# Optimization experiments

Hardware: AMD Instinct MI355X
Metric: run time of the kernel (lower is better)

Reference implementation:

```python
import jax, jax.numpy as jnp
import numpy as np

B, S, D_IN, D_OUT = 4, 4096, 768, 768

def setup_inputs() -> dict:
    key = jax.random.key(0)
    k1, k2, k3, k4 = jax.random.split(key, 4)
    x = jax.random.normal(k1, (B, S, D_IN), dtype=jnp.float32)
    # Stored as [d_in, d_out]; torch Linear computes x @ W.T with W [d_out, d_in],
    # which is equivalent to x @ W_here for a fresh random init.
    Wq = jax.random.normal(k2, (D_IN, D_OUT), dtype=jnp.float32) * (1.0 / np.sqrt(D_IN))
    Wk = jax.random.normal(k3, (D_IN, D_OUT), dtype=jnp.float32) * (1.0 / np.sqrt(D_IN))
    Wv = jax.random.normal(k4, (D_IN, D_OUT), dtype=jnp.float32) * (1.0 / np.sqrt(D_IN))
    return {"x": x, "Wq": Wq, "Wk": Wk, "Wv": Wv}

def reference(x, Wq, Wk, Wv):
    # x: [B, S, d_in]
    q = jnp.einsum('bsi,io->bso', x, Wq)  # [B, S, d_out]
    k = jnp.einsum('bsi,io->bso', x, Wk)
    v = jnp.einsum('bsi,io->bso', x, Wv)
    scale = 1.0 / jnp.sqrt(jnp.asarray(q.shape[-1], dtype=q.dtype))
    scores = jnp.einsum('bqd,bkd->bqk', q, k)  # [B, S, S]
    S_len = scores.shape[-1]
    causal = jnp.tril(jnp.ones((S_len, S_len), dtype=bool))  # True = keep
    scores = jnp.where(causal[None, :, :], scores, -jnp.inf)
    weights = jax.nn.softmax(scores * scale, axis=-1)
    # dropout p=0.0 -> identity
    return jnp.einsum('bqk,bkd->bqd', weights, v)
```

## Files before the change

### kernel.cpp

```cpp
#include <hip/hip_runtime.h>

typedef __attribute__((ext_vector_type(8))) short short8;
typedef __attribute__((ext_vector_type(4))) float f32x4;
typedef unsigned short u16;

#define MFMA_BF16 __builtin_amdgcn_mfma_f32_16x16x32_bf16
#define S_BARRIER()  asm volatile("s_barrier" ::: "memory")
#define WAIT_LGKM0() asm volatile("s_waitcnt lgkmcnt(0)" ::: "memory")
#define WAIT_VM(n)   asm volatile("s_waitcnt vmcnt(" #n ")" ::: "memory")

__device__ __forceinline__ u16 f2bf(float f) {
    unsigned int u = __builtin_bit_cast(unsigned int, f);
    u = (u + 0x7FFFu + ((u >> 16) & 1u)) >> 16;
    return (u16)u;
}

__device__ __forceinline__ void gl_lds16(const void* g, void* l) {
    __builtin_amdgcn_global_load_lds(
        (const __attribute__((address_space(1))) unsigned int*)g,
        (__attribute__((address_space(3))) unsigned int*)l, 16, 0, 0);
}

constexpr int D = 768;
constexpr int S = 4096;
constexpr float SCALE = 0.03608439182435161f;

__device__ __forceinline__ void tri_decode(int t, int& i, int& j) {
    i = (int)((sqrtf(8.0f * t + 1.0f) - 1.0f) * 0.5f);
    while ((i + 1) * (i + 2) / 2 <= t) ++i;
    while (i * (i + 1) / 2 > t) --i;
    j = t - i * (i + 1) / 2;
}

template<int NCH>
__device__ __forceinline__ void stage64(const u16* __restrict__ g, u16* lds, int kcol, int tid) {
    #pragma unroll
    for (int i = 0; i < NCH; ++i) {
        const int ch = i * 512 + tid;
        const int row = ch >> 3, c = ch & 7;
        const int cs = c ^ (row & 7);
        gl_lds16(g + (size_t)row * 768 + kcol + cs * 8, lds + ch * 8);
    }
}
__device__ __forceinline__ short8 ldsfrag(const u16* p, int row, int ks, int lane) {
    const int cs = (ks * 4 + (lane >> 4)) ^ (row & 7);
    return *reinterpret_cast<const short8*>(p + row * 64 + cs * 8);
}

__global__ __launch_bounds__(256)
void conv_x(const float* __restrict__ x, u16* __restrict__ xb) {
    const size_t i = ((size_t)blockIdx.x * 256 + threadIdx.x) * 4;
    const float4 v = *reinterpret_cast<const float4*>(x + i);
    ushort4 o;
    o.x = f2bf(v.x); o.y = f2bf(v.y); o.z = f2bf(v.z); o.w = f2bf(v.w);
    *reinterpret_cast<ushort4*>(xb + i) = o;
}

__global__ __launch_bounds__(256)
void conv_wt(const float* __restrict__ Wq, const float* __restrict__ Wk,
             const float* __restrict__ Wv, u16* __restrict__ WT) {
    __shared__ float t[64][65];
    const int tid = threadIdx.x;
    const int k0 = blockIdx.x * 64, n0 = blockIdx.y * 64, z = blockIdx.z;
    const float* __restrict__ W = (z == 0) ? Wq : ((z == 1) ? Wk : Wv);
    #pragma unroll
    for (int i = 0; i < 4; ++i) {
        const int e = (i * 256 + tid) * 4;
        const int r = e >> 6, c = e & 63;
        const float4 v = *reinterpret_cast<const float4*>(W + (size_t)(k0 + r) * D + n0 + c);
        t[r][c] = v.x; t[r][c + 1] = v.y; t[r][c + 2] = v.z; t[r][c + 3] = v.w;
    }
    __syncthreads();
    u16* O = WT + (size_t)z * D * D;
    #pragma unroll
    for (int i = 0; i < 4; ++i) {
        const int e = (i * 256 + tid) * 4;
        const int n = e >> 6, kq = e & 63;
        ushort4 o;
        o.x = f2bf(t[kq + 0][n]); o.y = f2bf(t[kq + 1][n]);
        o.z = f2bf(t[kq + 2][n]); o.w = f2bf(t[kq + 3][n]);
        *reinterpret_cast<ushort4*>(O + (size_t)(n0 + n) * D + k0 + kq) = o;
    }
}

__global__ __launch_bounds__(512)
void qkv_gemm(const u16* __restrict__ xb, const u16* __restrict__ WT,
              u16* __restrict__ qo, u16* __restrict__ ko, u16* __restrict__ vb)
{
    __shared__ u16 sAb[2 * 256 * 64];
    __shared__ u16 sBb[2 * 192 * 64];
    const int tid = threadIdx.x, lane = tid & 63, w = tid >> 6;
    const int wr = w >> 2, wn = w & 3;
    const int bm = blockIdx.x * 256;
    const u16* __restrict__ A = xb + (size_t)bm * 768;
    const u16* __restrict__ B = WT + (size_t)blockIdx.y * 192 * 768;

    f32x4 acc[8][3] = {};

    stage64<4>(A, sAb, 0, tid);  stage64<3>(B, sBb, 0, tid);
    stage64<4>(A, sAb + 16384, 64, tid);  stage64<3>(B, sBb + 12288, 64, tid);
    WAIT_VM(7); S_BARRIER();

    #pragma unroll 2
    for (int kt = 0; kt < 12; ++kt) {
        const int cur = kt & 1;
        const u16* pA = sAb + cur * 16384;
        const u16* pB = sBb + cur * 12288;
        short8 a0[8], b0[3], a1[8], b1[3];
        #pragma unroll
        for (int fr = 0; fr < 8; ++fr) a0[fr] = ldsfrag(pA, wr * 128 + fr * 16 + (lane & 15), 0, lane);
        #pragma unroll
        for (int fc = 0; fc < 3; ++fc) b0[fc] = ldsfrag(pB, wn * 48 + fc * 16 + (lane & 15), 0, lane);
        #pragma unroll
        for (int fr = 0; fr < 8; ++fr)
            #pragma unroll
            for (int fc = 0; fc < 3; ++fc)
                acc[fr][fc] = MFMA_BF16(a0[fr], b0[fc], acc[fr][fc], 0, 0, 0);
        #pragma unroll
        for (int fr = 0; fr < 8; ++fr) a1[fr] = ldsfrag(pA, wr * 128 + fr * 16 + (lane & 15), 1, lane);
        #pragma unroll
        for (int fc = 0; fc < 3; ++fc) b1[fc] = ldsfrag(pB, wn * 48 + fc * 16 + (lane & 15), 1, lane);
        WAIT_LGKM0(); S_BARRIER();
        if (kt < 10) { stage64<4>(A, sAb + cur * 16384, (kt + 2) * 64, tid);
                       stage64<3>(B, sBb + cur * 12288, (kt + 2) * 64, tid); }
        __builtin_amdgcn_s_setprio(1);
        #pragma unroll
        for (int fr = 0; fr < 8; ++fr)
            #pragma unroll
            for (int fc = 0; fc < 3; ++fc)
                acc[fr][fc] = MFMA_BF16(a1[fr], b1[fc], acc[fr][fc], 0, 0, 0);
        __builtin_amdgcn_s_setprio(0);
        if (kt < 10) { WAIT_VM(7); } else { WAIT_VM(0); }
        S_BARRIER();
    }

    const int z = blockIdx.y >> 2, nb = (blockIdx.y & 3) * 192;
    u16* __restrict__ dst = (z == 0) ? qo : ((z == 1) ? ko : vb);
    #pragma unroll
    for (int fr = 0; fr < 8; ++fr)
        #pragma unroll
        for (int fc = 0; fc < 3; ++fc)
            #pragma unroll
            for (int r = 0; r < 4; ++r) {
                const int m = bm + wr * 128 + fr * 16 + (lane >> 4) * 4 + r;
                const int n = nb + wn * 48 + fc * 16 + (lane & 15);
                dst[(size_t)m * 768 + n] = f2bf(acc[fr][fc][r]);
            }
}

__global__ __launch_bounds__(256)
void tr_v(const u16* __restrict__ vb, u16* __restrict__ vt)
{
    __shared__ u16 t[64 * 64];
    const int tid = threadIdx.x;
    const int s0 = blockIdx.x * 64, d0 = blockIdx.y * 64, b = blockIdx.z;
    const u16* __restrict__ src = vb + ((size_t)b * 4096 + s0) * 768 + d0;
    #pragma unroll
    for (int i = 0; i < 2; ++i) {
        const int ch = i * 256 + tid, r = ch >> 3, c = ch & 7;
        const int pc = c ^ ((r >> 3) & 7);
        *reinterpret_cast<short8*>(&t[r * 64 + pc * 8]) =
            *reinterpret_cast<const short8*>(src + (size_t)r * 768 + c * 8);
    }
    __syncthreads();
    u16* __restrict__ dstp = vt + ((size_t)b * 768 + d0) * 4096 + s0;
    #pragma unroll
    for (int i = 0; i < 2; ++i) {
        const int ch = i * 256 + tid, dd = ch >> 3, sc = ch & 7;
        short8 o;
        #pragma unroll
        for (int e = 0; e < 8; ++e)
            o[e] = (short)t[(sc * 8 + e) * 64 + (((dd >> 3) ^ sc) & 7) * 8 + (dd & 7)];
        *reinterpret_cast<short8*>(dstp + (size_t)dd * 4096 + sc * 8) = o;
    }
}

__global__ __launch_bounds__(512, 4)
void qkt_gemm(const u16* __restrict__ Qg, const u16* __restrict__ Kg,
              u16* __restrict__ Pp, float* __restrict__ Lp)
{
    __shared__ u16 smem[32768];
    const int tid = threadIdx.x, lane = tid & 63, w = tid >> 6;
    const int wr = w >> 2, wn = w & 3;
    int ti, tj;
    tri_decode(blockIdx.x, ti, tj);
    const int b = blockIdx.y;
    const u16* __restrict__ A = Qg + ((size_t)b * S + ti * 128) * 768;
    const u16* __restrict__ B = Kg + ((size_t)b * S + tj * 128) * 768;

    f32x4 acc[4][2] = {};

    stage64<2>(A, smem, 0, tid);           stage64<2>(B, smem + 16384, 0, tid);
    stage64<2>(A, smem + 8192, 64, tid);   stage64<2>(B, smem + 24576, 64, tid);
    WAIT_VM(4); S_BARRIER();

    #pragma unroll 2
    for (int kt = 0; kt < 12; ++kt) {
        const int cur = kt & 1;
        const u16* pA = smem + cur * 8192;
        const u16* pB = smem + 16384 + cur * 8192;
        short8 a0[4], b0[2], a1[4], b1[2];
        #pragma unroll
        for (int fr = 0; fr < 4; ++fr) a0[fr] = ldsfrag(pA, wr * 64 + fr * 16 + (lane & 15), 0, lane);
        #pragma unroll
        for (int fc = 0; fc < 2; ++fc) b0[fc] = ldsfrag(pB, wn * 32 + fc * 16 + (lane & 15), 0, lane);
        #pragma unroll
        for (int fr = 0; fr < 4; ++fr)
            #pragma unroll
            for (int fc = 0; fc < 2; ++fc)
                acc[fr][fc] = MFMA_BF16(a0[fr], b0[fc], acc[fr][fc], 0, 0, 0);
        #pragma unroll
        for (int fr = 0; fr < 4; ++fr) a1[fr] = ldsfrag(pA, wr * 64 + fr * 16 + (lane & 15), 1, lane);
        #pragma unroll
        for (int fc = 0; fc < 2; ++fc) b1[fc] = ldsfrag(pB, wn * 32 + fc * 16 + (lane & 15), 1, lane);
        WAIT_LGKM0(); S_BARRIER();
        if (kt < 10) { stage64<2>(A, smem + cur * 8192, (kt + 2) * 64, tid);
                       stage64<2>(B, smem + 16384 + cur * 8192, (kt + 2) * 64, tid); }
        __builtin_amdgcn_s_setprio(1);
        #pragma unroll
        for (int fr = 0; fr < 4; ++fr)
            #pragma unroll
            for (int fc = 0; fc < 2; ++fc)
                acc[fr][fc] = MFMA_BF16(a1[fr], b1[fc], acc[fr][fc], 0, 0, 0);
        __builtin_amdgcn_s_setprio(0);
        if (kt < 10) { WAIT_VM(4); } else { WAIT_VM(0); }
        S_BARRIER();
    }

    u16* sC = smem;
    const bool diag = (ti == tj);
    #pragma unroll
    for (int fr = 0; fr < 4; ++fr)
        #pragma unroll
        for (int r = 0; r < 4; ++r) {
            const int ml = wr * 64 + fr * 16 + (lane >> 4) * 4 + r;
            const int gm = ti * 128 + ml;
            float rs = 0.0f;
            #pragma unroll
            for (int fc = 0; fc < 2; ++fc) {
                const int nl = wn * 32 + fc * 16 + (lane & 15);
                float p = __expf(acc[fr][fc][r] * SCALE - 10.0f);
                if (diag && (tj * 128 + nl) > gm) p = 0.0f;
                rs += p;
                sC[ml * 132 + nl] = f2bf(p);
            }
            rs += __shfl_xor(rs, 1);
            rs += __shfl_xor(rs, 2);
            rs += __shfl_xor(rs, 4);
            rs += __shfl_xor(rs, 8);
            if ((lane & 15) == 0)
                Lp[((size_t)b * 128 + tj * 4 + wn) * 4096 + gm] = rs;
        }
    __syncthreads();
    u16* __restrict__ tbase = Pp + ((size_t)b * 528 + (size_t)ti * (ti + 1) / 2 + tj) * 16384;
    #pragma unroll
    for (int v = 0; v < 4; ++v) {
        const int ch = v * 512 + tid;
        const int row = ch >> 4, c = ch & 15;
        const short8 o = *reinterpret_cast<const short8*>(&sC[row * 132 + c * 8]);
        *reinterpret_cast<short8*>(tbase + row * 128 + c * 8) = o;
    }
}

__global__ __launch_bounds__(256)
void reduce_l(const float* __restrict__ Lp, float* __restrict__ Li)
{
    const int row = blockIdx.x * 256 + threadIdx.x;
    const int b = row >> 12, r = row & 4095;
    const int jm = 4 * (r >> 7) + 3;
    float l = 0.0f;
    for (int j = 0; j <= jm; ++j)
        l += Lp[((size_t)b * 128 + j) * 4096 + r];
    Li[row] = 1.0f / l;
}

__global__ __launch_bounds__(512)
void pv_gemm(const u16* __restrict__ Pp, const u16* __restrict__ Vt,
             const float* __restrict__ Li, float* __restrict__ out)
{
    __shared__ u16 sV[2][192 * 64];
    __shared__ u16 sP[2][128 * 64];
    const int tid  = threadIdx.x;
    const int lane = tid & 63;
    const int w    = tid >> 6;
    const int wq   = w >> 2;
    const int wd   = w & 3;
    const int bid  = blockIdx.x;
    const int i    = 31 - (bid >> 4);
    const int b    = (bid >> 2) & 3;
    const int dq   = bid & 3;
    const int q0   = i * 128, d0 = dq * 192;
    const int nkt  = 2 * i + 2;
    const u16* __restrict__ Pt  = Pp + ((size_t)b * 528 + (size_t)i * (i + 1) / 2) * 16384;
    const u16* __restrict__ vtb = Vt + ((size_t)b * D + d0) * S;

    f32x4 acc[4][3] = {};

    auto stage_v = [&](int buf, int kt) {
        #pragma unroll
        for (int n = 0; n < 3; ++n) {
            const int ch  = n * 512 + tid;
            const int row = ch >> 3;
            const int csw = (ch & 7) ^ (row & 7);
            gl_lds16(vtb + (size_t)row * S + kt * 64 + csw * 8, &sV[buf][ch * 8]);
        }
    };
    auto stage_p = [&](int buf, int kt) {
        const u16* base = Pt + (size_t)(kt >> 1) * 16384 + (kt & 1) * 64;
        #pragma unroll
        for (int n = 0; n < 2; ++n) {
            const int ch  = n * 512 + tid;
            const int row = ch >> 3;
            const int csw = (ch & 7) ^ (row & 7);
            gl_lds16(base + row * 128 + csw * 8, &sP[buf][ch * 8]);
        }
    };

    stage_v(0, 0); stage_p(0, 0);
    __syncthreads();
    int cur = 0;
    for (int kt = 0; kt < nkt; ++kt) {
        if (kt + 1 < nkt) { stage_v(cur ^ 1, kt + 1); stage_p(cur ^ 1, kt + 1); }
        #pragma unroll
        for (int ks = 0; ks < 2; ++ks) {
            short8 a[4];
            #pragma unroll
            for (int fr = 0; fr < 4; ++fr) {
                const int row = wq * 64 + fr * 16 + (lane & 15);
                const int cch = (ks * 4 + (lane >> 4)) ^ (row & 7);
                a[fr] = *reinterpret_cast<const short8*>(&sP[cur][row * 64 + cch * 8]);
            }
            #pragma unroll
            for (int fc = 0; fc < 3; ++fc) {
                const int dr  = wd * 48 + fc * 16 + (lane & 15);
                const int vch = (ks * 4 + (lane >> 4)) ^ (dr & 7);
                const short8 bv = *reinterpret_cast<const short8*>(&sV[cur][dr * 64 + vch * 8]);
                #pragma unroll
                for (int fr = 0; fr < 4; ++fr)
                    acc[fr][fc] = MFMA_BF16(a[fr], bv, acc[fr][fc], 0, 0, 0);
            }
        }
        __syncthreads();
        cur ^= 1;
    }

    #pragma unroll
    for (int fr = 0; fr < 4; ++fr)
        #pragma unroll
        for (int rr = 0; rr < 4; ++rr) {
            const int row = q0 + wq * 64 + fr * 16 + (lane >> 4) * 4 + rr;
            const float linv = Li[b * 4096 + row];
            #pragma unroll
            for (int fc = 0; fc < 3; ++fc) {
                const int col = d0 + wd * 48 + fc * 16 + (lane & 15);
                out[((size_t)b * S + row) * D + col] = acc[fr][fc][rr] * linv;
            }
        }
}

extern "C" void kernel_launch(void* const* d_in, const int* in_sizes, int n_in,
                              void* d_out, int out_size, void* d_ws, size_t ws_size,
                              hipStream_t stream) {
    const float* x  = (const float*)d_in[0];
    const float* Wq = (const float*)d_in[1];
    const float* Wk = (const float*)d_in[2];
    const float* Wv = (const float*)d_in[3];
    float* out = (float*)d_out;

    const size_t SD = (size_t)16384 * 768;
    u16* q  = (u16*)d_ws;
    u16* k  = q  + SD;
    u16* vt = k  + SD;
    u16* xb = vt + SD;
    u16* WT = xb + SD;
    u16* Pp = WT + (size_t)3 * 768 * 768;
    u16* vb = Pp;
    float* Lp = (float*)(Pp + (size_t)4 * 528 * 16384);
    float* Li = Lp + (size_t)4 * 128 * 4096;
    (void)in_sizes; (void)n_in; (void)out_size; (void)ws_size;

    conv_x  <<<12288, 256, 0, stream>>>(x, xb);
    conv_wt <<<dim3(12, 12, 3), 256, 0, stream>>>(Wq, Wk, Wv, WT);
    qkv_gemm<<<dim3(64, 12), 512, 0, stream>>>(xb, WT, q, k, vb);
    tr_v    <<<dim3(64, 12, 4), 256, 0, stream>>>(vb, vt);
    qkt_gemm<<<dim3(528, 4), 512, 0, stream>>>(q, k, Pp, Lp);
    reduce_l<<<64, 256, 0, stream>>>(Lp, Li);
    pv_gemm <<<512, 512, 0, stream>>>(Pp, vt, Li, out);
}
```

Baseline: 295.8 us.

## Fuse V transpose into QKV GEMM epilogue and retile QK^T to 4 waves

The V output of the QKV GEMM is now transposed through LDS inside the GEMM epilogue and written straight to the transposed layout. This removes the separate tr_v kernel and its round trip of V through global memory. The QK^T kernel moves from 8 waves with 4x2 fragments to 4 waves with 4x4 fragments per wave, halving the partial row-sum slices that reduce_l must sum. Its triangular tile index is also remapped to spread neighbouring blocks. The larger per-wave tile raises register pressure, and the LDS transpose adds a barrier to the GEMM epilogue.

```diff
diff --git a/kernel.cpp b/kernel.cpp
--- a/kernel.cpp
+++ b/kernel.cpp
@@ -32,11 +32,11 @@
     j = t - i * (i + 1) / 2;
 }
 
-template<int NCH>
-__device__ __forceinline__ void stage64(const u16* __restrict__ g, u16* lds, int kcol, int tid) {
+template<int NCH, int NT>
+__device__ __forceinline__ void stageT(const u16* __restrict__ g, u16* lds, int kcol, int tid) {
     #pragma unroll
     for (int i = 0; i < NCH; ++i) {
-        const int ch = i * 512 + tid;
+        const int ch = i * NT + tid;
         const int row = ch >> 3, c = ch & 7;
         const int cs = c ^ (row & 7);
         gl_lds16(g + (size_t)row * 768 + kcol + cs * 8, lds + ch * 8);
@@ -85,10 +85,11 @@
 
 __global__ __launch_bounds__(512)
 void qkv_gemm(const u16* __restrict__ xb, const u16* __restrict__ WT,
-              u16* __restrict__ qo, u16* __restrict__ ko, u16* __restrict__ vb)
+              u16* __restrict__ qo, u16* __restrict__ ko, u16* __restrict__ vt)
 {
-    __shared__ u16 sAb[2 * 256 * 64];
-    __shared__ u16 sBb[2 * 192 * 64];
+    __shared__ u16 smem[57344];
+    u16* sAb = smem;
+    u16* sBb = smem + 32768;
     const int tid = threadIdx.x, lane = tid & 63, w = tid >> 6;
     const int wr = w >> 2, wn = w & 3;
     const int bm = blockIdx.x * 256;
@@ -97,8 +98,8 @@
 
     f32x4 acc[8][3] = {};
 
-    stage64<4>(A, sAb, 0, tid);  stage64<3>(B, sBb, 0, tid);
-    stage64<4>(A, sAb + 16384, 64, tid);  stage64<3>(B, sBb + 12288, 64, tid);
+    stageT<4,512>(A, sAb, 0, tid);  stageT<3,512>(B, sBb, 0, tid);
+    stageT<4,512>(A, sAb + 16384, 64, tid);  stageT<3,512>(B, sBb + 12288, 64, tid);
     WAIT_VM(7); S_BARRIER();
 
     #pragma unroll 2
@@ -121,8 +122,8 @@
         #pragma unroll
         for (int fc = 0; fc < 3; ++fc) b1[fc] = ldsfrag(pB, wn * 48 + fc * 16 + (lane & 15), 1, lane);
         WAIT_LGKM0(); S_BARRIER();
-        if (kt < 10) { stage64<4>(A, sAb + cur * 16384, (kt + 2) * 64, tid);
-                       stage64<3>(B, sBb + cur * 12288, (kt + 2) * 64, tid); }
+        if (kt < 10) { stageT<4,512>(A, sAb + cur * 16384, (kt + 2) * 64, tid);
+                       stageT<3,512>(B, sBb + cur * 12288, (kt + 2) * 64, tid); }
         __builtin_amdgcn_s_setprio(1);
         #pragma unroll
         for (int fr = 0; fr < 8; ++fr)
@@ -135,95 +136,96 @@
     }
 
     const int z = blockIdx.y >> 2, nb = (blockIdx.y & 3) * 192;
-    u16* __restrict__ dst = (z == 0) ? qo : ((z == 1) ? ko : vb);
-    #pragma unroll
-    for (int fr = 0; fr < 8; ++fr)
-        #pragma unroll
-        for (int fc = 0; fc < 3; ++fc)
-            #pragma unroll
-            for (int r = 0; r < 4; ++r) {
-                const int m = bm + wr * 128 + fr * 16 + (lane >> 4) * 4 + r;
-                const int n = nb + wn * 48 + fc * 16 + (lane & 15);
-                dst[(size_t)m * 768 + n] = f2bf(acc[fr][fc][r]);
-            }
-}
-
-__global__ __launch_bounds__(256)
-void tr_v(const u16* __restrict__ vb, u16* __restrict__ vt)
-{
-    __shared__ u16 t[64 * 64];
-    const int tid = threadIdx.x;
-    const int s0 = blockIdx.x * 64, d0 = blockIdx.y * 64, b = blockIdx.z;
-    const u16* __restrict__ src = vb + ((size_t)b * 4096 + s0) * 768 + d0;
-    #pragma unroll
-    for (int i = 0; i < 2; ++i) {
-        const int ch = i * 256 + tid, r = ch >> 3, c = ch & 7;
-        const int pc = c ^ ((r >> 3) & 7);
-        *reinterpret_cast<short8*>(&t[r * 64 + pc * 8]) =
-            *reinterpret_cast<const short8*>(src + (size_t)r * 768 + c * 8);
-    }
-    __syncthreads();
-    u16* __restrict__ dstp = vt + ((size_t)b * 768 + d0) * 4096 + s0;
-    #pragma unroll
-    for (int i = 0; i < 2; ++i) {
-        const int ch = i * 256 + tid, dd = ch >> 3, sc = ch & 7;
-        short8 o;
-        #pragma unroll
-        for (int e = 0; e < 8; ++e)
-            o[e] = (short)t[(sc * 8 + e) * 64 + (((dd >> 3) ^ sc) & 7) * 8 + (dd & 7)];
-        *reinterpret_cast<short8*>(dstp + (size_t)dd * 4096 + sc * 8) = o;
-    }
-}
-
-__global__ __launch_bounds__(512, 4)
+    if (z == 2) {
+        u16* sT = smem;
+        #pragma unroll
+        for (int fr = 0; fr < 8; ++fr)
+            #pragma unroll
+            for (int fc = 0; fc < 3; ++fc) {
+                const int n  = wn * 48 + fc * 16 + (lane & 15);
+                const int mb = wr * 128 + fr * 16 + (lane >> 4) * 4;
+                ushort4 pk;
+                pk.x = f2bf(acc[fr][fc][0]); pk.y = f2bf(acc[fr][fc][1]);
+                pk.z = f2bf(acc[fr][fc][2]); pk.w = f2bf(acc[fr][fc][3]);
+                *reinterpret_cast<ushort4*>(&sT[n * 256 + (mb ^ ((n & 7) << 3))]) = pk;
+            }
+        __syncthreads();
+        const int batch = bm >> 12, s_in = bm & 4095;
+        u16* __restrict__ vdst = vt + ((size_t)batch * 768 + nb) * 4096 + s_in;
+        #pragma unroll
+        for (int v = 0; v < 12; ++v) {
+            const int ch = v * 512 + tid;
+            const int dd = ch >> 5, sc = ch & 31;
+            const short8 o = *reinterpret_cast<const short8*>(
+                &sT[dd * 256 + ((sc * 8) ^ ((dd & 7) << 3))]);
+            *reinterpret_cast<short8*>(vdst + (size_t)dd * 4096 + sc * 8) = o;
+        }
+    } else {
+        u16* __restrict__ dst = (z == 0) ? qo : ko;
+        #pragma unroll
+        for (int fr = 0; fr < 8; ++fr)
+            #pragma unroll
+            for (int fc = 0; fc < 3; ++fc)
+                #pragma unroll
+                for (int r = 0; r < 4; ++r) {
+                    const int m = bm + wr * 128 + fr * 16 + (lane >> 4) * 4 + r;
+                    const int n = nb + wn * 48 + fc * 16 + (lane & 15);
+                    dst[(size_t)m * 768 + n] = f2bf(acc[fr][fc][r]);
+                }
+    }
+}
+
+__global__ __launch_bounds__(256, 2)
 void qkt_gemm(const u16* __restrict__ Qg, const u16* __restrict__ Kg,
               u16* __restrict__ Pp, float* __restrict__ Lp)
 {
     __shared__ u16 smem[32768];
     const int tid = threadIdx.x, lane = tid & 63, w = tid >> 6;
-    const int wr = w >> 2, wn = w & 3;
+    const int wr = w >> 1, wn = w & 1;
+    const int bx = blockIdx.x;
+    const int bxs = (bx & 7) * 66 + (bx >> 3);
     int ti, tj;
-    tri_decode(blockIdx.x, ti, tj);
+    tri_decode(bxs, ti, tj);
     const int b = blockIdx.y;
     const u16* __restrict__ A = Qg + ((size_t)b * S + ti * 128) * 768;
     const u16* __restrict__ B = Kg + ((size_t)b * S + tj * 128) * 768;
 
-    f32x4 acc[4][2] = {};
-
-    stage64<2>(A, smem, 0, tid);           stage64<2>(B, smem + 16384, 0, tid);
-    stage64<2>(A, smem + 8192, 64, tid);   stage64<2>(B, smem + 24576, 64, tid);
-    WAIT_VM(4); S_BARRIER();
+    f32x4 acc[4][4] = {};
+
+    stageT<4,256>(A, smem, 0, tid);           stageT<4,256>(B, smem + 16384, 0, tid);
+    stageT<4,256>(A, smem + 8192, 64, tid);   stageT<4,256>(B, smem + 24576, 64, tid);
+    WAIT_VM(8); S_BARRIER();
 
     #pragma unroll 2
     for (int kt = 0; kt < 12; ++kt) {
         const int cur = kt & 1;
         const u16* pA = smem + cur * 8192;
         const u16* pB = smem + 16384 + cur * 8192;
-        short8 a0[4], b0[2], a1[4], b1[2];
+        short8 a0[4], b0[4], a1[4], b1[4];
         #pragma unroll
         for (int fr = 0; fr < 4; ++fr) a0[fr] = ldsfrag(pA, wr * 64 + fr * 16 + (lane & 15), 0, lane);
         #pragma unroll
-        for (int fc = 0; fc < 2; ++fc) b0[fc] = ldsfrag(pB, wn * 32 + fc * 16 + (lane & 15), 0, lane);
+        for (int fc = 0; fc < 4; ++fc) b0[fc] = ldsfrag(pB, wn * 64 + fc * 16 + (lane & 15), 0, lane);
         #pragma unroll
         for (int fr = 0; fr < 4; ++fr)
             #pragma unroll
-            for (int fc = 0; fc < 2; ++fc)
+            for (int fc = 0; fc < 4; ++fc)
                 acc[fr][fc] = MFMA_BF16(a0[fr], b0[fc], acc[fr][fc], 0, 0, 0);
         #pragma unroll
         for (int fr = 0; fr < 4; ++fr) a1[fr] = ldsfrag(pA, wr * 64 + fr * 16 + (lane & 15), 1, lane);
         #pragma unroll
-        for (int fc = 0; fc < 2; ++fc) b1[fc] = ldsfrag(pB, wn * 32 + fc * 16 + (lane & 15), 1, lane);
+        for (int fc = 0; fc < 4; ++fc) b1[fc] = ldsfrag(pB, wn * 64 + fc * 16 + (lane & 15), 1, lane);
         WAIT_LGKM0(); S_BARRIER();
-        if (kt < 10) { stage64<2>(A, smem + cur * 8192, (kt + 2) * 64, tid);
-                       stage64<2>(B, smem + 16384 + cur * 8192, (kt + 2) * 64, tid); }
+        if (kt < 10) { stageT<4,256>(A, smem + cur * 8192, (kt + 2) * 64, tid);
+                       stageT<4,256>(B, smem + 16384 + cur * 8192, (kt + 2) * 64, tid); }
         __builtin_amdgcn_s_setprio(1);
         #pragma unroll
         for (int fr = 0; fr < 4; ++fr)
             #pragma unroll
-            for (int fc = 0; fc < 2; ++fc)
+            for (int fc = 0; fc < 4; ++fc)
                 acc[fr][fc] = MFMA_BF16(a1[fr], b1[fc], acc[fr][fc], 0, 0, 0);
         __builtin_amdgcn_s_setprio(0);
-        if (kt < 10) { WAIT_VM(4); } else { WAIT_VM(0); }
+        if (kt < 10) { WAIT_VM(8); } else { WAIT_VM(0); }
         S_BARRIER();
     }
 
@@ -237,8 +239,8 @@
             const int gm = ti * 128 + ml;
             float rs = 0.0f;
             #pragma unroll
-            for (int fc = 0; fc < 2; ++fc) {
-                const int nl = wn * 32 + fc * 16 + (lane & 15);
+            for (int fc = 0; fc < 4; ++fc) {
+                const int nl = wn * 64 + fc * 16 + (lane & 15);
                 float p = __expf(acc[fr][fc][r] * SCALE - 10.0f);
                 if (diag && (tj * 128 + nl) > gm) p = 0.0f;
                 rs += p;
@@ -249,13 +251,13 @@
             rs += __shfl_xor(rs, 4);
             rs += __shfl_xor(rs, 8);
             if ((lane & 15) == 0)
-                Lp[((size_t)b * 128 + tj * 4 + wn) * 4096 + gm] = rs;
+                Lp[((size_t)b * 64 + tj * 2 + wn) * 4096 + gm] = rs;
         }
     __syncthreads();
     u16* __restrict__ tbase = Pp + ((size_t)b * 528 + (size_t)ti * (ti + 1) / 2 + tj) * 16384;
     #pragma unroll
-    for (int v = 0; v < 4; ++v) {
-        const int ch = v * 512 + tid;
+    for (int v = 0; v < 8; ++v) {
+        const int ch = v * 256 + tid;
         const int row = ch >> 4, c = ch & 15;
         const short8 o = *reinterpret_cast<const short8*>(&sC[row * 132 + c * 8]);
         *reinterpret_cast<short8*>(tbase + row * 128 + c * 8) = o;
@@ -267,10 +269,10 @@
 {
     const int row = blockIdx.x * 256 + threadIdx.x;
     const int b = row >> 12, r = row & 4095;
-    const int jm = 4 * (r >> 7) + 3;
+    const int jm = 2 * (r >> 7) + 1;
     float l = 0.0f;
     for (int j = 0; j <= jm; ++j)
-        l += Lp[((size_t)b * 128 + j) * 4096 + r];
+        l += Lp[((size_t)b * 64 + j) * 4096 + r];
     Li[row] = 1.0f / l;
 }
 
@@ -374,16 +376,14 @@
     u16* xb = vt + SD;
     u16* WT = xb + SD;
     u16* Pp = WT + (size_t)3 * 768 * 768;
-    u16* vb = Pp;
     float* Lp = (float*)(Pp + (size_t)4 * 528 * 16384);
-    float* Li = Lp + (size_t)4 * 128 * 4096;
+    float* Li = Lp + (size_t)4 * 64 * 4096;
     (void)in_sizes; (void)n_in; (void)out_size; (void)ws_size;
 
     conv_x  <<<12288, 256, 0, stream>>>(x, xb);
     conv_wt <<<dim3(12, 12, 3), 256, 0, stream>>>(Wq, Wk, Wv, WT);
-    qkv_gemm<<<dim3(64, 12), 512, 0, stream>>>(xb, WT, q, k, vb);
-    tr_v    <<<dim3(64, 12, 4), 256, 0, stream>>>(vb, vt);
-    qkt_gemm<<<dim3(528, 4), 512, 0, stream>>>(q, k, Pp, Lp);
+    qkv_gemm<<<dim3(64, 12), 512, 0, stream>>>(xb, WT, q, k, vt);
+    qkt_gemm<<<dim3(528, 4), 256, 0, stream>>>(q, k, Pp, Lp);
     reduce_l<<<64, 256, 0, stream>>>(Lp, Li);
     pv_gemm <<<512, 512, 0, stream>>>(Pp, vt, Li, out);
 }
```

Measured after the change: 260.1 us. -12.1%, faster.
